# Kernel tuning notes

Hardware: AMD Instinct MI355X
Metric: run time of the kernel (lower is better)

## Reference

```python
import jax, jax.numpy as jnp
import numpy as np

EPS_LN = 1e-5   # torch.nn.LayerNorm default eps
EPS_Q = 1e-5    # BitNetQuantizer eps
QMAX = 127.0    # 2**(8-1) - 1 for 8-bit activations


def _layernorm(v):
    # LayerNorm without affine params, biased variance (torch default)
    mu = jnp.mean(v, axis=-1, keepdims=True)
    var = jnp.var(v, axis=-1, keepdims=True)
    return (v - mu) / jnp.sqrt(var + EPS_LN)


def setup_inputs() -> dict:
    key = jax.random.key(0)
    k1, k2, k3 = jax.random.split(key, 3)
    B, S, DIN, DOUT = 4, 4096, 2048, 2048
    x = jax.random.normal(k1, (B, S, DIN), dtype=jnp.float32)
    # ternary weights in {-1, 0, +1}
    weight_ternary = jax.random.randint(k2, (DOUT, DIN), -1, 2, dtype=jnp.int32)
    # positive per-row scale (from_float uses a scalar expanded; per-row is the stored form)
    weight_scale = jax.random.uniform(k3, (DOUT,), dtype=jnp.float32, minval=0.01, maxval=0.05)
    return {"x": x, "weight_ternary": weight_ternary, "weight_scale": weight_scale}


def reference(x, weight_ternary, weight_scale):
    # input LayerNorm (no affine)
    xn = _layernorm(x)
    # 8-bit activation quantization: per-token absmax scale
    x_scale = jnp.clip(jnp.max(jnp.abs(xn), axis=-1, keepdims=True), EPS_Q, None) / QMAX
    x_quant = jnp.clip(jnp.round(xn / x_scale), -QMAX, QMAX)
    x_float = x_quant * x_scale  # [B, S, DIN]
    # dequantize ternary weights: [DOUT, DIN]
    w = weight_ternary.astype(jnp.float32) * weight_scale[:, None]
    # F.linear: x @ w.T
    out = jnp.einsum('bsi,oi->bso', x_float, w)
    # output LayerNorm (no affine)
    return _layernorm(out)
```

## Files before the change

### kernel.cpp

```cpp
#include <hip/hip_runtime.h>
#include <hip/hip_bf16.h>
#include <stdint.h>

using int32x4 = __attribute__((ext_vector_type(4))) int;

#define DIN 2048
#define DOUT 2048
#define NTOK 16384
#define KDIM 2048
#define NDIM 2048

#define BM 256
#define BN 256
#define BKB 64
#define NKT (KDIM / BKB)
#define TILEB (BM * BKB)

typedef const __attribute__((address_space(1))) void* gp_t;
typedef __attribute__((address_space(3))) void* lp_t;

__device__ __forceinline__ void gload16(const void* g, void* l) {
    __builtin_amdgcn_global_load_lds((gp_t)g, (lp_t)l, 16, 0, 0);
}

__global__ __launch_bounds__(256) void k_wconv(const int* __restrict__ wt,
                                               signed char* __restrict__ w8) {
    int i = blockIdx.x * 256 + threadIdx.x;
    int4 v = ((const int4*)wt)[i];
    char4 c;
    c.x = (signed char)v.x; c.y = (signed char)v.y;
    c.z = (signed char)v.z; c.w = (signed char)v.w;
    ((char4*)w8)[i] = c;
}

__global__ __launch_bounds__(256) void k_lnq(const float* __restrict__ x,
                                             signed char* __restrict__ xq,
                                             float* __restrict__ xscale) {
    __shared__ float sm[12];
    const int row = blockIdx.x;
    const int tid = threadIdx.x;
    const float* p = x + (size_t)row * DIN;
    const float4 v0 = ((const float4*)p)[tid * 2];
    const float4 v1 = ((const float4*)p)[tid * 2 + 1];
    float vv[8] = {v0.x, v0.y, v0.z, v0.w, v1.x, v1.y, v1.z, v1.w};
    float s = 0.f, ss = 0.f;
#pragma unroll
    for (int i = 0; i < 8; i++) { s += vv[i]; ss += vv[i] * vv[i]; }
#pragma unroll
    for (int o = 32; o; o >>= 1) { s += __shfl_down(s, o); ss += __shfl_down(ss, o); }
    const int wv = tid >> 6;
    if ((tid & 63) == 0) { sm[wv] = s; sm[4 + wv] = ss; }
    __syncthreads();
    s = sm[0] + sm[1] + sm[2] + sm[3];
    ss = sm[4] + sm[5] + sm[6] + sm[7];
    const float mu = s * (1.f / DIN);
    const float var = ss * (1.f / DIN) - mu * mu;
    const float rstd = 1.f / sqrtf(var + 1e-5f);
    float am = 0.f;
#pragma unroll
    for (int i = 0; i < 8; i++) am = fmaxf(am, fabsf(vv[i] - mu));
#pragma unroll
    for (int o = 32; o; o >>= 1) am = fmaxf(am, __shfl_down(am, o));
    __syncthreads();
    if ((tid & 63) == 0) sm[8 + wv] = am;
    __syncthreads();
    am = fmaxf(fmaxf(sm[8], sm[9]), fmaxf(sm[10], sm[11]));
    const float scale = fmaxf(am * rstd, 1e-5f) * (1.f / 127.f);
    union { signed char c[8]; int2 v; } u;
#pragma unroll
    for (int i = 0; i < 8; i++) {
        float xn = (vv[i] - mu) * rstd;
        float t = rintf(xn / scale);
        t = fminf(127.f, fmaxf(-127.f, t));
        u.c[i] = (signed char)t;
    }
    ((int2*)(xq + (size_t)row * DIN))[tid] = u.v;
    if (tid == 0) xscale[row] = scale;
}

#define MFMA4(I, AF) \
    acc[I][0] = __builtin_amdgcn_mfma_i32_16x16x64_i8(AF, b0, acc[I][0], 0, 0, 0); \
    acc[I][1] = __builtin_amdgcn_mfma_i32_16x16x64_i8(AF, b1, acc[I][1], 0, 0, 0); \
    acc[I][2] = __builtin_amdgcn_mfma_i32_16x16x64_i8(AF, b2, acc[I][2], 0, 0, 0); \
    acc[I][3] = __builtin_amdgcn_mfma_i32_16x16x64_i8(AF, b3, acc[I][3], 0, 0, 0);

#define SCHED __builtin_amdgcn_sched_barrier(0);
#define BAR   __builtin_amdgcn_s_barrier();

template <bool B16OUT>
__global__ __launch_bounds__(512, 2) void k_gemm(const signed char* __restrict__ A,
                                                 const signed char* __restrict__ B,
                                                 const float* __restrict__ xs,
                                                 const float* __restrict__ wsc,
                                                 void* __restrict__ Cout) {
    __shared__ __align__(16) signed char lA[3][TILEB];
    __shared__ __align__(16) signed char lB[3][TILEB];
    __shared__ float s_xs[BM];
    __shared__ float s_ws[BN];

    const int tid = threadIdx.x;
    const int orig = blockIdx.x;
    const int bid = (orig & 7) * 64 + (orig >> 3);
    const int bm = bid >> 3;
    const int bn = bid & 7;

    const int lane = tid & 63;
    const int wave = tid >> 6;
    const int wm = wave >> 2;
    const int wn = wave & 3;
    const int lo = lane & 15;
    const int q  = lane >> 4;

    const int srow = tid >> 2;
    const int gch  = (tid & 3) ^ ((srow >> 1) & 3);
    const signed char* gA = A + (size_t)(bm * BM + srow) * KDIM + gch * 16;
    const signed char* gB = B + (size_t)(bn * BN + srow) * KDIM + gch * 16;
    const int dst = tid * 16;

    const int slot = (q ^ ((lo >> 1) & 3)) * 16;
    const int abase = (wm * 128 + lo) * BKB + slot;
    const int bbase = (wn * 64 + lo) * BKB + slot;

    if (tid < 256) s_xs[tid] = xs[bm * BM + tid];
    else           s_ws[tid - 256] = wsc[bn * BN + tid - 256];

#define STAGE_A(T, BUF) \
    gload16(gA + (T) * BKB,                      &lA[BUF][0] + dst); \
    gload16(gA + (T) * BKB + (size_t)128 * KDIM, &lA[BUF][0] + dst + 8192);
#define STAGE_B(T, BUF) \
    gload16(gB + (T) * BKB,                      &lB[BUF][0] + dst); \
    gload16(gB + (T) * BKB + (size_t)128 * KDIM, &lB[BUF][0] + dst + 8192);

    STAGE_A(0, 0) STAGE_B(0, 0)
    STAGE_A(1, 1) STAGE_B(1, 1)
    asm volatile("s_waitcnt vmcnt(0)" ::: "memory");
    SCHED BAR SCHED

    int32x4 acc[8][4];
#pragma unroll
    for (int i = 0; i < 8; i++)
#pragma unroll
        for (int j = 0; j < 4; j++) {
            int32x4 z = {0, 0, 0, 0};
            acc[i][j] = z;
        }

    int cur = 0, nx2 = 2;
    for (int t = 0; t < NKT; ++t) {
        const signed char* lAc = &lA[cur][0];
        const signed char* lBc = &lB[cur][0];
        int32x4 a0, a1, a2, a3, a4, a5, a6, a7, b0, b1, b2, b3;

        a0 = *(const int32x4*)(lAc + abase + 0 * 1024);
        a1 = *(const int32x4*)(lAc + abase + 1 * 1024);
        a2 = *(const int32x4*)(lAc + abase + 2 * 1024);
        a3 = *(const int32x4*)(lAc + abase + 3 * 1024);
        b0 = *(const int32x4*)(lBc + bbase + 0 * 1024);
        b1 = *(const int32x4*)(lBc + bbase + 1 * 1024);
        b2 = *(const int32x4*)(lBc + bbase + 2 * 1024);
        b3 = *(const int32x4*)(lBc + bbase + 3 * 1024);
        a4 = *(const int32x4*)(lAc + abase + 4 * 1024);
        a5 = *(const int32x4*)(lAc + abase + 5 * 1024);
        a6 = *(const int32x4*)(lAc + abase + 6 * 1024);
        a7 = *(const int32x4*)(lAc + abase + 7 * 1024);
        asm volatile("s_waitcnt vmcnt(0)" ::: "memory");
        SCHED
        BAR
        SCHED
        if (t + 2 < NKT) {
            STAGE_A(t + 2, nx2)
            STAGE_B(t + 2, nx2)
        }
        SCHED
        asm volatile("s_waitcnt lgkmcnt(4)" ::: "memory");
        SCHED
        __builtin_amdgcn_s_setprio(1);
        MFMA4(0, a0) MFMA4(1, a1) MFMA4(2, a2) MFMA4(3, a3)
        __builtin_amdgcn_s_setprio(0);
        SCHED
        asm volatile("s_waitcnt lgkmcnt(0)" ::: "memory");
        SCHED
        __builtin_amdgcn_s_setprio(1);
        MFMA4(4, a4) MFMA4(5, a5) MFMA4(6, a6) MFMA4(7, a7)
        __builtin_amdgcn_s_setprio(0);
        SCHED

        cur = (cur == 2) ? 0 : cur + 1;
        nx2 = (nx2 == 2) ? 0 : nx2 + 1;
    }

#pragma unroll
    for (int i = 0; i < 8; ++i) {
#pragma unroll
        for (int j = 0; j < 4; ++j) {
            const int ln = wn * 64 + j * 16 + lo;
            const float wsv = s_ws[ln];
            const size_t base = (size_t)(bm * BM + wm * 128 + i * 16 + q * 4) * NDIM + bn * BN + ln;
#pragma unroll
            for (int r = 0; r < 4; ++r) {
                const int lm = wm * 128 + i * 16 + q * 4 + r;
                const float v = (float)acc[i][j][r] * s_xs[lm] * wsv;
                if constexpr (B16OUT) {
                    ((__hip_bfloat16*)Cout)[base + (size_t)r * NDIM] = __float2bfloat16(v);
                } else {
                    ((float*)Cout)[base + (size_t)r * NDIM] = v;
                }
            }
        }
    }
}

__global__ __launch_bounds__(256) void k_lnout_b(const __hip_bfloat16* __restrict__ cb,
                                                 float* __restrict__ y) {
    __shared__ float sm[8];
    const int row = blockIdx.x;
    const int tid = threadIdx.x;
    int4 raw = ((const int4*)(cb + (size_t)row * DOUT))[tid];
    union { int4 v; unsigned u[4]; } U; U.v = raw;
    float vv[8];
#pragma unroll
    for (int k = 0; k < 4; k++) {
        vv[2 * k]     = __uint_as_float(U.u[k] << 16);
        vv[2 * k + 1] = __uint_as_float(U.u[k] & 0xffff0000u);
    }
    float s = 0.f, ss = 0.f;
#pragma unroll
    for (int i = 0; i < 8; i++) { s += vv[i]; ss += vv[i] * vv[i]; }
#pragma unroll
    for (int o = 32; o; o >>= 1) { s += __shfl_down(s, o); ss += __shfl_down(ss, o); }
    const int wv = tid >> 6;
    if ((tid & 63) == 0) { sm[wv] = s; sm[4 + wv] = ss; }
    __syncthreads();
    s = sm[0] + sm[1] + sm[2] + sm[3];
    ss = sm[4] + sm[5] + sm[6] + sm[7];
    const float mu = s * (1.f / DOUT);
    const float var = ss * (1.f / DOUT) - mu * mu;
    const float rstd = 1.f / sqrtf(var + 1e-5f);
    float* p = y + (size_t)row * DOUT;
    float4 o0, o1;
    o0.x = (vv[0] - mu) * rstd; o0.y = (vv[1] - mu) * rstd;
    o0.z = (vv[2] - mu) * rstd; o0.w = (vv[3] - mu) * rstd;
    o1.x = (vv[4] - mu) * rstd; o1.y = (vv[5] - mu) * rstd;
    o1.z = (vv[6] - mu) * rstd; o1.w = (vv[7] - mu) * rstd;
    ((float4*)p)[tid * 2] = o0;
    ((float4*)p)[tid * 2 + 1] = o1;
}

__global__ __launch_bounds__(256) void k_lnout(float* __restrict__ y) {
    __shared__ float sm[8];
    const int row = blockIdx.x;
    const int tid = threadIdx.x;
    float* p = y + (size_t)row * DOUT;
    float4 v0 = ((float4*)p)[tid * 2];
    float4 v1 = ((float4*)p)[tid * 2 + 1];
    float vv[8] = {v0.x, v0.y, v0.z, v0.w, v1.x, v1.y, v1.z, v1.w};
    float s = 0.f, ss = 0.f;
#pragma unroll
    for (int i = 0; i < 8; i++) { s += vv[i]; ss += vv[i] * vv[i]; }
#pragma unroll
    for (int o = 32; o; o >>= 1) { s += __shfl_down(s, o); ss += __shfl_down(ss, o); }
    const int wv = tid >> 6;
    if ((tid & 63) == 0) { sm[wv] = s; sm[4 + wv] = ss; }
    __syncthreads();
    s = sm[0] + sm[1] + sm[2] + sm[3];
    ss = sm[4] + sm[5] + sm[6] + sm[7];
    const float mu = s * (1.f / DOUT);
    const float var = ss * (1.f / DOUT) - mu * mu;
    const float rstd = 1.f / sqrtf(var + 1e-5f);
#pragma unroll
    for (int i = 0; i < 8; i++) vv[i] = (vv[i] - mu) * rstd;
    float4 o0, o1;
    o0.x = vv[0]; o0.y = vv[1]; o0.z = vv[2]; o0.w = vv[3];
    o1.x = vv[4]; o1.y = vv[5]; o1.z = vv[6]; o1.w = vv[7];
    ((float4*)p)[tid * 2] = o0;
    ((float4*)p)[tid * 2 + 1] = o1;
}

extern "C" void kernel_launch(void* const* d_in, const int* in_sizes, int n_in,
                              void* d_out, int out_size, void* d_ws, size_t ws_size,
                              hipStream_t stream) {
    const float* x = (const float*)d_in[0];
    const int* wt = (const int*)d_in[1];
    const float* wscale = (const float*)d_in[2];
    float* out = (float*)d_out;

    signed char* w8 = (signed char*)d_ws;
    signed char* xq = (signed char*)d_ws + (size_t)4 * 1024 * 1024;
    float* xs = (float*)((char*)d_ws + (size_t)36 * 1024 * 1024);
    __hip_bfloat16* c16 = (__hip_bfloat16*)((char*)d_ws + (size_t)40 * 1024 * 1024);
    const bool use16 = ws_size >= (size_t)104 * 1024 * 1024;

    k_wconv<<<(DOUT * DIN / 4) / 256, 256, 0, stream>>>(wt, w8);
    k_lnq<<<NTOK, 256, 0, stream>>>(x, xq, xs);
    if (use16) {
        k_gemm<true><<<(NTOK / BM) * (NDIM / BN), 512, 0, stream>>>(xq, w8, xs, wscale, (void*)c16);
        k_lnout_b<<<NTOK, 256, 0, stream>>>(c16, out);
    } else {
        k_gemm<false><<<(NTOK / BM) * (NDIM / BN), 512, 0, stream>>>(xq, w8, xs, wscale, (void*)out);
        k_lnout<<<NTOK, 256, 0, stream>>>(out);
    }
}
```

Measured before the change: 151.0 us.

## Load B fragments directly from global into registers, drop B LDS staging

The GEMM no longer stages the weight (B) tile through shared memory. Each wave loads its B fragments straight from global memory into double-buffered registers one k-step ahead. The A tile moves to a 4-deep LDS ring, and the main loop is unrolled by four so the buffer indices are compile-time constants. This cuts LDS traffic and LDS footprint, but each wave now issues its own uncoalesced 16-byte global loads for B, duplicated across the two wm waves, and register pressure rises under the 2-blocks-per-CU launch bound.

```diff
diff --git a/kernel.cpp b/kernel.cpp
--- a/kernel.cpp
+++ b/kernel.cpp
@@ -78,14 +78,14 @@
     if (tid == 0) xscale[row] = scale;
 }
 
-#define MFMA4(I, AF) \
-    acc[I][0] = __builtin_amdgcn_mfma_i32_16x16x64_i8(AF, b0, acc[I][0], 0, 0, 0); \
-    acc[I][1] = __builtin_amdgcn_mfma_i32_16x16x64_i8(AF, b1, acc[I][1], 0, 0, 0); \
-    acc[I][2] = __builtin_amdgcn_mfma_i32_16x16x64_i8(AF, b2, acc[I][2], 0, 0, 0); \
-    acc[I][3] = __builtin_amdgcn_mfma_i32_16x16x64_i8(AF, b3, acc[I][3], 0, 0, 0);
-
 #define SCHED __builtin_amdgcn_sched_barrier(0);
 #define BAR   __builtin_amdgcn_s_barrier();
+
+#define MFMA4S(I, AF, S) \
+    acc[I][0] = __builtin_amdgcn_mfma_i32_16x16x64_i8(AF, b##S##0, acc[I][0], 0, 0, 0); \
+    acc[I][1] = __builtin_amdgcn_mfma_i32_16x16x64_i8(AF, b##S##1, acc[I][1], 0, 0, 0); \
+    acc[I][2] = __builtin_amdgcn_mfma_i32_16x16x64_i8(AF, b##S##2, acc[I][2], 0, 0, 0); \
+    acc[I][3] = __builtin_amdgcn_mfma_i32_16x16x64_i8(AF, b##S##3, acc[I][3], 0, 0, 0);
 
 template <bool B16OUT>
 __global__ __launch_bounds__(512, 2) void k_gemm(const signed char* __restrict__ A,
@@ -93,8 +93,7 @@
                                                  const float* __restrict__ xs,
                                                  const float* __restrict__ wsc,
                                                  void* __restrict__ Cout) {
-    __shared__ __align__(16) signed char lA[3][TILEB];
-    __shared__ __align__(16) signed char lB[3][TILEB];
+    __shared__ __align__(16) signed char lA[4][TILEB];
     __shared__ float s_xs[BM];
     __shared__ float s_ws[BN];
 
@@ -114,12 +113,12 @@
     const int srow = tid >> 2;
     const int gch  = (tid & 3) ^ ((srow >> 1) & 3);
     const signed char* gA = A + (size_t)(bm * BM + srow) * KDIM + gch * 16;
-    const signed char* gB = B + (size_t)(bn * BN + srow) * KDIM + gch * 16;
     const int dst = tid * 16;
 
     const int slot = (q ^ ((lo >> 1) & 3)) * 16;
     const int abase = (wm * 128 + lo) * BKB + slot;
-    const int bbase = (wn * 64 + lo) * BKB + slot;
+
+    const signed char* gBr = B + (size_t)(bn * BN + wn * 64 + lo) * KDIM + q * 16;
 
     if (tid < 256) s_xs[tid] = xs[bm * BM + tid];
     else           s_ws[tid - 256] = wsc[bn * BN + tid - 256];
@@ -127,12 +126,17 @@
 #define STAGE_A(T, BUF) \
     gload16(gA + (T) * BKB,                      &lA[BUF][0] + dst); \
     gload16(gA + (T) * BKB + (size_t)128 * KDIM, &lA[BUF][0] + dst + 8192);
-#define STAGE_B(T, BUF) \
-    gload16(gB + (T) * BKB,                      &lB[BUF][0] + dst); \
-    gload16(gB + (T) * BKB + (size_t)128 * KDIM, &lB[BUF][0] + dst + 8192);
-
-    STAGE_A(0, 0) STAGE_B(0, 0)
-    STAGE_A(1, 1) STAGE_B(1, 1)
+#define LOADB(S, T) \
+    b##S##0 = *(const int32x4*)(gBr + (size_t)(T) * BKB + 0 * 16 * KDIM); \
+    b##S##1 = *(const int32x4*)(gBr + (size_t)(T) * BKB + 1 * 16 * KDIM); \
+    b##S##2 = *(const int32x4*)(gBr + (size_t)(T) * BKB + 2 * 16 * KDIM); \
+    b##S##3 = *(const int32x4*)(gBr + (size_t)(T) * BKB + 3 * 16 * KDIM);
+
+    int32x4 bX0, bX1, bX2, bX3, bY0, bY1, bY2, bY3;
+    int32x4 a0, a1, a2, a3, a4, a5, a6, a7;
+
+    STAGE_A(0, 0) STAGE_A(1, 1)
+    LOADB(X, 0)
     asm volatile("s_waitcnt vmcnt(0)" ::: "memory");
     SCHED BAR SCHED
 
@@ -145,48 +149,40 @@
             acc[i][j] = z;
         }
 
-    int cur = 0, nx2 = 2;
-    for (int t = 0; t < NKT; ++t) {
-        const signed char* lAc = &lA[cur][0];
-        const signed char* lBc = &lB[cur][0];
-        int32x4 a0, a1, a2, a3, a4, a5, a6, a7, b0, b1, b2, b3;
-
-        a0 = *(const int32x4*)(lAc + abase + 0 * 1024);
-        a1 = *(const int32x4*)(lAc + abase + 1 * 1024);
-        a2 = *(const int32x4*)(lAc + abase + 2 * 1024);
-        a3 = *(const int32x4*)(lAc + abase + 3 * 1024);
-        b0 = *(const int32x4*)(lBc + bbase + 0 * 1024);
-        b1 = *(const int32x4*)(lBc + bbase + 1 * 1024);
-        b2 = *(const int32x4*)(lBc + bbase + 2 * 1024);
-        b3 = *(const int32x4*)(lBc + bbase + 3 * 1024);
-        a4 = *(const int32x4*)(lAc + abase + 4 * 1024);
-        a5 = *(const int32x4*)(lAc + abase + 5 * 1024);
-        a6 = *(const int32x4*)(lAc + abase + 6 * 1024);
-        a7 = *(const int32x4*)(lAc + abase + 7 * 1024);
-        asm volatile("s_waitcnt vmcnt(0)" ::: "memory");
-        SCHED
-        BAR
-        SCHED
-        if (t + 2 < NKT) {
-            STAGE_A(t + 2, nx2)
-            STAGE_B(t + 2, nx2)
-        }
-        SCHED
-        asm volatile("s_waitcnt lgkmcnt(4)" ::: "memory");
-        SCHED
-        __builtin_amdgcn_s_setprio(1);
-        MFMA4(0, a0) MFMA4(1, a1) MFMA4(2, a2) MFMA4(3, a3)
-        __builtin_amdgcn_s_setprio(0);
-        SCHED
-        asm volatile("s_waitcnt lgkmcnt(0)" ::: "memory");
-        SCHED
-        __builtin_amdgcn_s_setprio(1);
-        MFMA4(4, a4) MFMA4(5, a5) MFMA4(6, a6) MFMA4(7, a7)
-        __builtin_amdgcn_s_setprio(0);
-        SCHED
-
-        cur = (cur == 2) ? 0 : cur + 1;
-        nx2 = (nx2 == 2) ? 0 : nx2 + 1;
+#define ITER(T, CS, NS, CUR, STG) { \
+    const signed char* lAc = &lA[CUR][0]; \
+    a0 = *(const int32x4*)(lAc + abase + 0 * 1024); \
+    a1 = *(const int32x4*)(lAc + abase + 1 * 1024); \
+    a2 = *(const int32x4*)(lAc + abase + 2 * 1024); \
+    a3 = *(const int32x4*)(lAc + abase + 3 * 1024); \
+    a4 = *(const int32x4*)(lAc + abase + 4 * 1024); \
+    a5 = *(const int32x4*)(lAc + abase + 5 * 1024); \
+    a6 = *(const int32x4*)(lAc + abase + 6 * 1024); \
+    a7 = *(const int32x4*)(lAc + abase + 7 * 1024); \
+    asm volatile("s_waitcnt vmcnt(0)" ::: "memory"); \
+    SCHED BAR SCHED \
+    if ((T) + 2 < NKT) { STAGE_A((T) + 2, STG) } \
+    if ((T) + 1 < NKT) { LOADB(NS, (T) + 1) } \
+    SCHED \
+    asm volatile("s_waitcnt lgkmcnt(4)" ::: "memory"); \
+    SCHED \
+    __builtin_amdgcn_s_setprio(1); \
+    MFMA4S(0, a0, CS) MFMA4S(1, a1, CS) MFMA4S(2, a2, CS) MFMA4S(3, a3, CS) \
+    __builtin_amdgcn_s_setprio(0); \
+    SCHED \
+    asm volatile("s_waitcnt lgkmcnt(0)" ::: "memory"); \
+    SCHED \
+    __builtin_amdgcn_s_setprio(1); \
+    MFMA4S(4, a4, CS) MFMA4S(5, a5, CS) MFMA4S(6, a6, CS) MFMA4S(7, a7, CS) \
+    __builtin_amdgcn_s_setprio(0); \
+    SCHED \
+}
+
+    for (int t = 0; t < NKT; t += 4) {
+        ITER(t + 0, X, Y, 0, 2)
+        ITER(t + 1, Y, X, 1, 3)
+        ITER(t + 2, X, Y, 2, 0)
+        ITER(t + 3, Y, X, 3, 1)
     }
 
 #pragma unroll
```

Measured after the change: 196.6 us. +30.2%, slower.

## Double-buffer 128-wide K tiles with interleaved prefetch and fuse weight conversion

Applied to the files above, without the earlier changes.

The GEMM main loop moves from a triple-buffered 64-byte K tile to a double-buffered 128-byte K tile. LDS reads use a new 8-chunk XOR swizzle, and global-to-LDS prefetches of the next tile are split across four MFMA phases separated by barriers. Separately, the int32-to-int8 weight conversion is folded into the first blocks of the LayerNorm-quantize kernel, which removes one kernel launch. The extra barriers and the tighter vmcnt waits could add stalls, while the larger K step halves the number of loop iterations and buffer switches.

```diff
diff --git a/kernel.cpp b/kernel.cpp
--- a/kernel.cpp
+++ b/kernel.cpp
@@ -12,7 +12,7 @@
 
 #define BM 256
 #define BN 256
-#define BKB 64
+#define BKB 128
 #define NKT (KDIM / BKB)
 #define TILEB (BM * BKB)
 
@@ -23,22 +23,24 @@
     __builtin_amdgcn_global_load_lds((gp_t)g, (lp_t)l, 16, 0, 0);
 }
 
-__global__ __launch_bounds__(256) void k_wconv(const int* __restrict__ wt,
-                                               signed char* __restrict__ w8) {
-    int i = blockIdx.x * 256 + threadIdx.x;
-    int4 v = ((const int4*)wt)[i];
-    char4 c;
-    c.x = (signed char)v.x; c.y = (signed char)v.y;
-    c.z = (signed char)v.z; c.w = (signed char)v.w;
-    ((char4*)w8)[i] = c;
-}
-
 __global__ __launch_bounds__(256) void k_lnq(const float* __restrict__ x,
                                              signed char* __restrict__ xq,
-                                             float* __restrict__ xscale) {
+                                             float* __restrict__ xscale,
+                                             const int* __restrict__ wt,
+                                             signed char* __restrict__ w8) {
     __shared__ float sm[12];
     const int row = blockIdx.x;
     const int tid = threadIdx.x;
+
+    if (row < (DOUT * DIN / 4) / 256) {
+        const int i = row * 256 + tid;
+        int4 v = ((const int4*)wt)[i];
+        char4 c;
+        c.x = (signed char)v.x; c.y = (signed char)v.y;
+        c.z = (signed char)v.z; c.w = (signed char)v.w;
+        ((char4*)w8)[i] = c;
+    }
+
     const float* p = x + (size_t)row * DIN;
     const float4 v0 = ((const float4*)p)[tid * 2];
     const float4 v1 = ((const float4*)p)[tid * 2 + 1];
@@ -78,14 +80,15 @@
     if (tid == 0) xscale[row] = scale;
 }
 
-#define MFMA4(I, AF) \
-    acc[I][0] = __builtin_amdgcn_mfma_i32_16x16x64_i8(AF, b0, acc[I][0], 0, 0, 0); \
-    acc[I][1] = __builtin_amdgcn_mfma_i32_16x16x64_i8(AF, b1, acc[I][1], 0, 0, 0); \
-    acc[I][2] = __builtin_amdgcn_mfma_i32_16x16x64_i8(AF, b2, acc[I][2], 0, 0, 0); \
-    acc[I][3] = __builtin_amdgcn_mfma_i32_16x16x64_i8(AF, b3, acc[I][3], 0, 0, 0);
+#define MFMA4(I, AF, B0, B1, B2, B3) \
+    acc[I][0] = __builtin_amdgcn_mfma_i32_16x16x64_i8(AF, B0, acc[I][0], 0, 0, 0); \
+    acc[I][1] = __builtin_amdgcn_mfma_i32_16x16x64_i8(AF, B1, acc[I][1], 0, 0, 0); \
+    acc[I][2] = __builtin_amdgcn_mfma_i32_16x16x64_i8(AF, B2, acc[I][2], 0, 0, 0); \
+    acc[I][3] = __builtin_amdgcn_mfma_i32_16x16x64_i8(AF, B3, acc[I][3], 0, 0, 0);
 
 #define SCHED __builtin_amdgcn_sched_barrier(0);
 #define BAR   __builtin_amdgcn_s_barrier();
+#define LGKM0 asm volatile("s_waitcnt lgkmcnt(0)" ::: "memory"); SCHED
 
 template <bool B16OUT>
 __global__ __launch_bounds__(512, 2) void k_gemm(const signed char* __restrict__ A,
@@ -93,8 +96,8 @@
                                                  const float* __restrict__ xs,
                                                  const float* __restrict__ wsc,
                                                  void* __restrict__ Cout) {
-    __shared__ __align__(16) signed char lA[3][TILEB];
-    __shared__ __align__(16) signed char lB[3][TILEB];
+    __shared__ __align__(16) signed char lA[2][TILEB];
+    __shared__ __align__(16) signed char lB[2][TILEB];
     __shared__ float s_xs[BM];
     __shared__ float s_ws[BN];
 
@@ -111,30 +114,32 @@
     const int lo = lane & 15;
     const int q  = lane >> 4;
 
-    const int srow = tid >> 2;
-    const int gch  = (tid & 3) ^ ((srow >> 1) & 3);
-    const signed char* gA = A + (size_t)(bm * BM + srow) * KDIM + gch * 16;
-    const signed char* gB = B + (size_t)(bn * BN + srow) * KDIM + gch * 16;
-    const int dst = tid * 16;
-
-    const int slot = (q ^ ((lo >> 1) & 3)) * 16;
-    const int abase = (wm * 128 + lo) * BKB + slot;
-    const int bbase = (wn * 64 + lo) * BKB + slot;
+    const int srow = tid >> 3;
+    const int schunk = tid & 7;
+    const int gchunk = schunk ^ (srow & 7);
+    const signed char* gA = A + (size_t)(bm * BM + srow) * KDIM + gchunk * 16;
+    const signed char* gB = B + (size_t)(bn * BN + srow) * KDIM + gchunk * 16;
+    const int dst = srow * BKB + schunk * 16;
+
+    const int arow = (wm * 128 + lo) * BKB;
+    const int brow = (wn * 64 + lo) * BKB;
+    const int ck0 = (q ^ (lane & 7)) * 16;
+    const int ck1 = ((4 + q) ^ (lane & 7)) * 16;
 
     if (tid < 256) s_xs[tid] = xs[bm * BM + tid];
     else           s_ws[tid - 256] = wsc[bn * BN + tid - 256];
 
-#define STAGE_A(T, BUF) \
-    gload16(gA + (T) * BKB,                      &lA[BUF][0] + dst); \
-    gload16(gA + (T) * BKB + (size_t)128 * KDIM, &lA[BUF][0] + dst + 8192);
-#define STAGE_B(T, BUF) \
-    gload16(gB + (T) * BKB,                      &lB[BUF][0] + dst); \
-    gload16(gB + (T) * BKB + (size_t)128 * KDIM, &lB[BUF][0] + dst + 8192);
-
-    STAGE_A(0, 0) STAGE_B(0, 0)
-    STAGE_A(1, 1) STAGE_B(1, 1)
-    asm volatile("s_waitcnt vmcnt(0)" ::: "memory");
-    SCHED BAR SCHED
+#define GLA(KB, J, LDSP) gload16(gA + (KB) + (size_t)(J) * 64 * KDIM, (LDSP) + dst + (J) * 8192);
+#define GLB(KB, J, LDSP) gload16(gB + (KB) + (size_t)(J) * 64 * KDIM, (LDSP) + dst + (J) * 8192);
+
+    {
+        signed char* la0 = &lA[0][0];
+        signed char* lb0 = &lB[0][0];
+        GLA(0, 0, la0) GLA(0, 2, la0) GLB(0, 2, lb0) GLB(0, 3, lb0)
+        GLB(0, 0, lb0) GLB(0, 1, lb0) GLA(0, 1, la0) GLA(0, 3, la0)
+    }
+    asm volatile("s_waitcnt vmcnt(2)" ::: "memory");
+    BAR
 
     int32x4 acc[8][4];
 #pragma unroll
@@ -145,48 +150,72 @@
             acc[i][j] = z;
         }
 
-    int cur = 0, nx2 = 2;
     for (int t = 0; t < NKT; ++t) {
-        const signed char* lAc = &lA[cur][0];
-        const signed char* lBc = &lB[cur][0];
-        int32x4 a0, a1, a2, a3, a4, a5, a6, a7, b0, b1, b2, b3;
-
-        a0 = *(const int32x4*)(lAc + abase + 0 * 1024);
-        a1 = *(const int32x4*)(lAc + abase + 1 * 1024);
-        a2 = *(const int32x4*)(lAc + abase + 2 * 1024);
-        a3 = *(const int32x4*)(lAc + abase + 3 * 1024);
-        b0 = *(const int32x4*)(lBc + bbase + 0 * 1024);
-        b1 = *(const int32x4*)(lBc + bbase + 1 * 1024);
-        b2 = *(const int32x4*)(lBc + bbase + 2 * 1024);
-        b3 = *(const int32x4*)(lBc + bbase + 3 * 1024);
-        a4 = *(const int32x4*)(lAc + abase + 4 * 1024);
-        a5 = *(const int32x4*)(lAc + abase + 5 * 1024);
-        a6 = *(const int32x4*)(lAc + abase + 6 * 1024);
-        a7 = *(const int32x4*)(lAc + abase + 7 * 1024);
-        asm volatile("s_waitcnt vmcnt(0)" ::: "memory");
-        SCHED
+        const signed char* lAc = &lA[t & 1][0];
+        const signed char* lBc = &lB[t & 1][0];
+        signed char* lAn = &lA[(t + 1) & 1][0];
+        signed char* lBn = &lB[(t + 1) & 1][0];
+        const bool pf = (t + 1 < NKT);
+        const size_t kb = (size_t)(t + 1) * BKB;
+        int32x4 a0, a1, a2, a3, bx0, bx1, bx2, bx3, by0, by1, by2, by3;
+
+        a0 = *(const int32x4*)(lAc + arow + 0 * 2048 + ck0);
+        a1 = *(const int32x4*)(lAc + arow + 1 * 2048 + ck0);
+        a2 = *(const int32x4*)(lAc + arow + 2 * 2048 + ck0);
+        a3 = *(const int32x4*)(lAc + arow + 3 * 2048 + ck0);
+        bx0 = *(const int32x4*)(lBc + brow + 0 * 2048 + ck0);
+        bx1 = *(const int32x4*)(lBc + brow + 1 * 2048 + ck0);
+        bx2 = *(const int32x4*)(lBc + brow + 2 * 2048 + ck0);
+        bx3 = *(const int32x4*)(lBc + brow + 3 * 2048 + ck0);
+        if (pf) { GLA(kb, 0, lAn) GLA(kb, 2, lAn) GLB(kb, 2, lBn) GLB(kb, 3, lBn) }
+        BAR LGKM0
+        __builtin_amdgcn_s_setprio(1);
+        MFMA4(0, a0, bx0, bx1, bx2, bx3) MFMA4(1, a1, bx0, bx1, bx2, bx3)
+        MFMA4(2, a2, bx0, bx1, bx2, bx3) MFMA4(3, a3, bx0, bx1, bx2, bx3)
+        __builtin_amdgcn_s_setprio(0);
+        if (pf) { asm volatile("s_waitcnt vmcnt(4)" ::: "memory"); }
+        else    { asm volatile("s_waitcnt vmcnt(0)" ::: "memory"); }
         BAR
-        SCHED
-        if (t + 2 < NKT) {
-            STAGE_A(t + 2, nx2)
-            STAGE_B(t + 2, nx2)
-        }
-        SCHED
-        asm volatile("s_waitcnt lgkmcnt(4)" ::: "memory");
-        SCHED
+
+        a0 = *(const int32x4*)(lAc + arow + 4 * 2048 + ck0);
+        a1 = *(const int32x4*)(lAc + arow + 5 * 2048 + ck0);
+        a2 = *(const int32x4*)(lAc + arow + 6 * 2048 + ck0);
+        a3 = *(const int32x4*)(lAc + arow + 7 * 2048 + ck0);
+        if (pf) { GLB(kb, 0, lBn) GLB(kb, 1, lBn) }
+        BAR LGKM0
         __builtin_amdgcn_s_setprio(1);
-        MFMA4(0, a0) MFMA4(1, a1) MFMA4(2, a2) MFMA4(3, a3)
+        MFMA4(4, a0, bx0, bx1, bx2, bx3) MFMA4(5, a1, bx0, bx1, bx2, bx3)
+        MFMA4(6, a2, bx0, bx1, bx2, bx3) MFMA4(7, a3, bx0, bx1, bx2, bx3)
         __builtin_amdgcn_s_setprio(0);
-        SCHED
-        asm volatile("s_waitcnt lgkmcnt(0)" ::: "memory");
-        SCHED
+        BAR
+
+        a0 = *(const int32x4*)(lAc + arow + 0 * 2048 + ck1);
+        a1 = *(const int32x4*)(lAc + arow + 1 * 2048 + ck1);
+        a2 = *(const int32x4*)(lAc + arow + 2 * 2048 + ck1);
+        a3 = *(const int32x4*)(lAc + arow + 3 * 2048 + ck1);
+        by0 = *(const int32x4*)(lBc + brow + 0 * 2048 + ck1);
+        by1 = *(const int32x4*)(lBc + brow + 1 * 2048 + ck1);
+        by2 = *(const int32x4*)(lBc + brow + 2 * 2048 + ck1);
+        by3 = *(const int32x4*)(lBc + brow + 3 * 2048 + ck1);
+        if (pf) { GLA(kb, 1, lAn) GLA(kb, 3, lAn) }
+        BAR LGKM0
         __builtin_amdgcn_s_setprio(1);
-        MFMA4(4, a4) MFMA4(5, a5) MFMA4(6, a6) MFMA4(7, a7)
+        MFMA4(0, a0, by0, by1, by2, by3) MFMA4(1, a1, by0, by1, by2, by3)
+        MFMA4(2, a2, by0, by1, by2, by3) MFMA4(3, a3, by0, by1, by2, by3)
         __builtin_amdgcn_s_setprio(0);
-        SCHED
-
-        cur = (cur == 2) ? 0 : cur + 1;
-        nx2 = (nx2 == 2) ? 0 : nx2 + 1;
+        BAR
+
+        a0 = *(const int32x4*)(lAc + arow + 4 * 2048 + ck1);
+        a1 = *(const int32x4*)(lAc + arow + 5 * 2048 + ck1);
+        a2 = *(const int32x4*)(lAc + arow + 6 * 2048 + ck1);
+        a3 = *(const int32x4*)(lAc + arow + 7 * 2048 + ck1);
+        BAR LGKM0
+        __builtin_amdgcn_s_setprio(1);
+        MFMA4(4, a0, by0, by1, by2, by3) MFMA4(5, a1, by0, by1, by2, by3)
+        MFMA4(6, a2, by0, by1, by2, by3) MFMA4(7, a3, by0, by1, by2, by3)
+        __builtin_amdgcn_s_setprio(0);
+        if (pf) { asm volatile("s_waitcnt vmcnt(2)" ::: "memory"); }
+        BAR
     }
 
 #pragma unroll
@@ -290,8 +319,7 @@
     __hip_bfloat16* c16 = (__hip_bfloat16*)((char*)d_ws + (size_t)40 * 1024 * 1024);
     const bool use16 = ws_size >= (size_t)104 * 1024 * 1024;
 
-    k_wconv<<<(DOUT * DIN / 4) / 256, 256, 0, stream>>>(wt, w8);
-    k_lnq<<<NTOK, 256, 0, stream>>>(x, xq, xs);
+    k_lnq<<<NTOK, 256, 0, stream>>>(x, xq, xs, wt, w8);
     if (use16) {
         k_gemm<true><<<(NTOK / BM) * (NDIM / BN), 512, 0, stream>>>(xq, w8, xs, wscale, (void*)c16);
         k_lnout_b<<<NTOK, 256, 0, stream>>>(c16, out);
```

Result: slower. 155.0 us (+2.6%).
